# Performance work log

Measured on AMD Instinct MI355X. Metric: run time of the kernel, lower is better.

The kernel has to match this reference:

```python
import jax, jax.numpy as jnp
import numpy as np

B, N, K = 4, 8192, 32
C_IN, C_MID, C_OUT = 64, 64, 128


def _uniform(key, shape, fan_in):
    s = 1.0 / np.sqrt(fan_in).astype(np.float32)
    return jax.random.uniform(key, shape, minval=-s, maxval=s, dtype=jnp.float32)


def setup_inputs() -> dict:
    key = jax.random.key(0)
    ks = jax.random.split(key, 8)
    p = jax.random.normal(ks[0], (B, N, 3), dtype=jnp.float32)
    f = jax.random.normal(ks[1], (B, C_IN, N), dtype=jnp.float32)
    dp = jax.random.normal(ks[2], (B, 3, N, K), dtype=jnp.float32)
    fj = jax.random.normal(ks[3], (B, C_IN, N, K), dtype=jnp.float32)
    # Conv2d 1x1 weights (PyTorch default kaiming-uniform-ish fan-in init)
    W1 = _uniform(ks[4], (C_MID, C_IN + 3), C_IN + 3)
    b1 = _uniform(ks[5], (C_MID,), C_IN + 3)
    W2 = _uniform(ks[6], (C_OUT, C_MID), C_MID)
    b2 = _uniform(ks[7], (C_OUT,), C_MID)
    return {"p": p, "f": f, "dp": dp, "fj": fj, "W1": W1, "b1": b1, "W2": W2, "b2": b2}


def reference(p, f, dp, fj, W1, b1, W2, b2):
    # fj <- cat([dp, fj], dim=1): [B, 3+C_in, N, K]
    x = jnp.concatenate([dp, fj], axis=1)
    # 1x1 Conv2d + ReLU (norm is None in source), layer 1: [B, C_mid, N, K]
    h = jax.nn.relu(jnp.einsum('oc,bcnk->bonk', W1, x) + b1[None, :, None, None])
    # layer 2 (use_res=False, is_head=False -> ReLU on last layer too): [B, C_out, N, K]
    h = jax.nn.relu(jnp.einsum('oc,bcnk->bonk', W2, h) + b2[None, :, None, None])
    # max-pool over neighbor axis K: [B, C_out, N]
    return jnp.max(h, axis=-1)
```

## Files before the change

### kernel.cpp

```cpp
#include <hip/hip_runtime.h>
#include <hip/hip_bf16.h>
#include <stdint.h>

#define B_    4
#define N_    8192
#define K_    32
#define CX    67
#define CMID  64
#define COUT  128

#define CSTR  100
#define HSTR  72
#define TPG   8
#define NWG   1024

typedef __bf16 bf16_t;
typedef bf16_t bf16x8 __attribute__((ext_vector_type(8)));
typedef bf16_t bf16x4 __attribute__((ext_vector_type(4)));
typedef float  f32x4  __attribute__((ext_vector_type(4)));

__device__ __forceinline__ uint32_t pack2bf(float a, float b) {
    union { bf16_t h[2]; uint32_t u; } x;
    x.h[0] = (bf16_t)a; x.h[1] = (bf16_t)b;
    return x.u;
}

template<bool DIRECT>
__global__ __launch_bounds__(256, 2)
void sa_main(const float* __restrict__ dp, const float* __restrict__ fj,
             const float* __restrict__ W1, const float* __restrict__ b1,
             const float* __restrict__ W2, const float* __restrict__ b2,
             float* __restrict__ dst)
{
    __shared__ bf16_t smem[4 * 32 * CSTR + 4 * 16 * HSTR];

    const int tid  = threadIdx.x;
    const int wave = tid >> 6;
    const int lane = tid & 63;
    const int lrow = lane & 15;
    const int g    = lane >> 4;

    bf16_t* Xw = smem + wave * 32 * CSTR;
    bf16_t* Hw = smem + 4 * 32 * CSTR + wave * 16 * HSTR;

    const size_t plane = (size_t)N_ * K_;
    const int cr = lane >> 3;
    const int k0 = (lane & 7) << 2;

    float4 v[9];
    auto issue = [&](int Gi) {
        const int bb = Gi >> 11;
        const int nn = ((Gi & 2047) << 2) + wave;
        const size_t rbase = (size_t)nn * K_ + k0;
        const float* dpb = dp + (size_t)bb * 3  * plane + rbase;
        const float* fjb = fj + (size_t)bb * 64 * plane + rbase;
        #pragma unroll
        for (int j = 0; j < 9; ++j) {
            int c = j * 8 + cr;
            int cc = (c < CX) ? c : (CX - 1);
            const float* p = (cc < 3) ? dpb + (size_t)cc * plane
                                      : fjb + (size_t)(cc - 3) * plane;
            v[j] = *(const float4*)p;
        }
    };
    issue(blockIdx.x * TPG);

    for (int i = tid; i < 64 * 96; i += 256) {
        int o = i / 96, c = i - o * 96;
        smem[i] = (c < CX) ? (bf16_t)W1[o * CX + c] : (bf16_t)0.f;
    }
    __syncthreads();
    bf16x8 w1f[3][4];
    #pragma unroll
    for (int kc = 0; kc < 3; ++kc)
        #pragma unroll
        for (int rt = 0; rt < 4; ++rt)
            w1f[kc][rt] = *(const bf16x8*)&smem[(rt * 16 + lrow) * 96 + kc * 32 + g * 8];
    __syncthreads();
    for (int i = tid; i < 128 * 72; i += 256) {
        int o = i / 72, c = i - o * 72;
        smem[i] = (c < CMID) ? (bf16_t)W2[o * CMID + c] : (bf16_t)0.f;
    }
    __syncthreads();
    bf16x8 w2f[2][8];
    #pragma unroll
    for (int kc = 0; kc < 2; ++kc)
        #pragma unroll
        for (int ot = 0; ot < 8; ++ot)
            w2f[kc][ot] = *(const bf16x8*)&smem[(ot * 16 + lrow) * 72 + kc * 32 + g * 8];
    __syncthreads();
    for (int i = tid; i < 4 * 32 * CSTR; i += 256) smem[i] = (bf16_t)0.f;
    __syncthreads();

    f32x4 b1f[4];
    #pragma unroll
    for (int rt = 0; rt < 4; ++rt) b1f[rt] = *(const f32x4*)(b1 + rt * 16 + g * 4);
    float b2f[8];
    #pragma unroll
    for (int ot = 0; ot < 8; ++ot) b2f[ot] = b2[ot * 16 + lrow];

    #pragma unroll 1
    for (int t = 0; t < TPG; ++t) {
        const int G = blockIdx.x * TPG + t;
        const int b = G >> 11;
        const int n = ((G & 2047) << 2) + wave;

        #pragma unroll
        for (int j = 0; j < 9; ++j) {
            int c = j * 8 + cr;
            if (c < CX) {
                Xw[(k0 + 0) * CSTR + c] = (bf16_t)v[j].x;
                Xw[(k0 + 1) * CSTR + c] = (bf16_t)v[j].y;
                Xw[(k0 + 2) * CSTR + c] = (bf16_t)v[j].z;
                Xw[(k0 + 3) * CSTR + c] = (bf16_t)v[j].w;
            }
        }
        {
            int Gn = G + 1;
            if (Gn > 8191) Gn = 8191;
            issue(Gn);
        }

        float macc[8];
        #pragma unroll
        for (int i = 0; i < 8; ++i) macc[i] = -3e38f;

        #pragma unroll
        for (int ct = 0; ct < 2; ++ct) {
            const int col = ct * 16 + lrow;
            f32x4 acc1[4] = {};
            #pragma unroll
            for (int kc = 0; kc < 3; ++kc) {
                bf16x4 lo = *(const bf16x4*)&Xw[col * CSTR + kc * 32 + g * 8];
                bf16x4 hi = *(const bf16x4*)&Xw[col * CSTR + kc * 32 + g * 8 + 4];
                bf16x8 bfX = __builtin_shufflevector(lo, hi, 0, 1, 2, 3, 4, 5, 6, 7);
                #pragma unroll
                for (int rt = 0; rt < 4; ++rt)
                    acc1[rt] = __builtin_amdgcn_mfma_f32_16x16x32_bf16(w1f[kc][rt], bfX, acc1[rt], 0, 0, 0);
            }
            #pragma unroll
            for (int rt = 0; rt < 4; ++rt) {
                float h0 = fmaxf(acc1[rt][0] + b1f[rt][0], 0.f);
                float h1 = fmaxf(acc1[rt][1] + b1f[rt][1], 0.f);
                float h2 = fmaxf(acc1[rt][2] + b1f[rt][2], 0.f);
                float h3 = fmaxf(acc1[rt][3] + b1f[rt][3], 0.f);
                *(uint2*)&Hw[lrow * HSTR + rt * 16 + g * 4] =
                    make_uint2(pack2bf(h0, h1), pack2bf(h2, h3));
            }
            bf16x8 hb0 = *(const bf16x8*)&Hw[lrow * HSTR +  0 + g * 8];
            bf16x8 hb1 = *(const bf16x8*)&Hw[lrow * HSTR + 32 + g * 8];
            #pragma unroll
            for (int bt = 0; bt < 2; ++bt) {
                f32x4 a2[4] = {};
                #pragma unroll
                for (int o = 0; o < 4; ++o) {
                    a2[o] = __builtin_amdgcn_mfma_f32_16x16x32_bf16(hb0, w2f[0][bt * 4 + o], a2[o], 0, 0, 0);
                    a2[o] = __builtin_amdgcn_mfma_f32_16x16x32_bf16(hb1, w2f[1][bt * 4 + o], a2[o], 0, 0, 0);
                }
                #pragma unroll
                for (int o = 0; o < 4; ++o) {
                    float m = fmaxf(fmaxf(a2[o][0], a2[o][1]), fmaxf(a2[o][2], a2[o][3]));
                    macc[bt * 4 + o] = fmaxf(macc[bt * 4 + o], m);
                }
            }
        }

        #pragma unroll
        for (int ot = 0; ot < 8; ++ot) {
            float vv = macc[ot];
            vv = fmaxf(vv, __shfl_xor(vv, 16, 64));
            vv = fmaxf(vv, __shfl_xor(vv, 32, 64));
            macc[ot] = fmaxf(vv + b2f[ot], 0.f);
        }
        float va = (g == 0) ? macc[0] : (g == 1) ? macc[2] : (g == 2) ? macc[4] : macc[6];
        float vb = (g == 0) ? macc[1] : (g == 1) ? macc[3] : (g == 2) ? macc[5] : macc[7];
        const int ca = g * 32 + lrow;
        const int cb = g * 32 + 16 + lrow;
        if (DIRECT) {
            float* op = dst + (size_t)b * COUT * N_ + n;
            op[(size_t)ca * N_] = va;
            op[(size_t)cb * N_] = vb;
        } else {
            float* wp = dst + ((size_t)(b * N_ + n)) * COUT;
            wp[ca] = va;
            wp[cb] = vb;
        }
    }
}

__global__ __launch_bounds__(256)
void sa_transpose(const float* __restrict__ ws, float* __restrict__ out)
{
    __shared__ float tile[32][136];
    const int t  = threadIdx.x;
    const int i  = blockIdx.x;
    const int b  = i >> 8;
    const int n0 = (i & 255) << 5;

    const float* rp = ws + ((size_t)(b * N_ + n0)) * COUT;
    #pragma unroll
    for (int r = 0; r < 4; ++r) {
        int flat = (r * 256 + t) * 4;
        int nl = flat >> 7, c = flat & 127;
        float4 v = *(const float4*)(rp + (size_t)nl * COUT + c);
        *(float4*)&tile[nl][c] = v;
    }
    __syncthreads();
    float* op = out + (size_t)b * COUT * N_ + n0;
    const int nl4 = (t & 7) << 2;
    #pragma unroll
    for (int r2 = 0; r2 < 4; ++r2) {
        int c = r2 * 32 + (t >> 3);
        float4 o4;
        o4.x = tile[nl4 + 0][c];
        o4.y = tile[nl4 + 1][c];
        o4.z = tile[nl4 + 2][c];
        o4.w = tile[nl4 + 3][c];
        *(float4*)(op + (size_t)c * N_ + nl4) = o4;
    }
}

extern "C" void kernel_launch(void* const* d_in, const int* in_sizes, int n_in,
                              void* d_out, int out_size, void* d_ws, size_t ws_size,
                              hipStream_t stream) {
    const float* dp = (const float*)d_in[2];
    const float* fj = (const float*)d_in[3];
    const float* W1 = (const float*)d_in[4];
    const float* b1 = (const float*)d_in[5];
    const float* W2 = (const float*)d_in[6];
    const float* b2 = (const float*)d_in[7];
    float* out = (float*)d_out;

    const size_t ws_need = (size_t)B_ * N_ * COUT * sizeof(float);
    if (ws_size >= ws_need) {
        float* ws = (float*)d_ws;
        hipLaunchKernelGGL((sa_main<false>), dim3(NWG), dim3(256), 0, stream,
                           dp, fj, W1, b1, W2, b2, ws);
        hipLaunchKernelGGL(sa_transpose, dim3(1024), dim3(256), 0, stream, ws, out);
    } else {
        hipLaunchKernelGGL((sa_main<true>), dim3(NWG), dim3(256), 0, stream,
                           dp, fj, W1, b1, W2, b2, out);
    }
}
```

Measured before the change: 111.3 us.

## Double-buffer global loads two points ahead and add MFMA wave priority

The kernel now keeps two register buffers of input loads and prefetches two points ahead instead of one, so more global memory latency can be hidden behind MFMA work. The per-channel load address computation is simplified into strided pointer increments instead of per-element selects. s_setprio is raised around the MFMA blocks. The extra register buffer raises VGPR pressure, which at launch bounds 256,2 may cause spills.

Result: slower. 115.0 us (+3.3%).

```diff
diff --git a/kernel.cpp b/kernel.cpp
--- a/kernel.cpp
+++ b/kernel.cpp
@@ -13,6 +13,7 @@
 #define HSTR  72
 #define TPG   8
 #define NWG   1024
+#define GMAX  8191
 
 typedef __bf16 bf16_t;
 typedef bf16_t bf16x8 __attribute__((ext_vector_type(8)));
@@ -47,23 +48,31 @@
     const int cr = lane >> 3;
     const int k0 = (lane & 7) << 2;
 
-    float4 v[9];
-    auto issue = [&](int Gi) {
+    auto issue = [&](float4 (&v)[9], int Gi) {
         const int bb = Gi >> 11;
         const int nn = ((Gi & 2047) << 2) + wave;
         const size_t rbase = (size_t)nn * K_ + k0;
-        const float* dpb = dp + (size_t)bb * 3  * plane + rbase;
-        const float* fjb = fj + (size_t)bb * 64 * plane + rbase;
-        #pragma unroll
-        for (int j = 0; j < 9; ++j) {
-            int c = j * 8 + cr;
-            int cc = (c < CX) ? c : (CX - 1);
-            const float* p = (cc < 3) ? dpb + (size_t)cc * plane
-                                      : fjb + (size_t)(cc - 3) * plane;
-            v[j] = *(const float4*)p;
-        }
+        const float* fp  = fj + (size_t)bb * 64 * plane + rbase;
+        const float* dp0 = dp + (size_t)bb * 3  * plane + rbase;
+        const float* p0 = (cr < 3) ? dp0 + (size_t)cr * plane
+                                   : fp  + (size_t)(cr - 3) * plane;
+        v[0] = *(const float4*)p0;
+        const float* pj = fp + (size_t)(8 + cr - 3) * plane;
+        #pragma unroll
+        for (int j = 1; j < 8; ++j) {
+            v[j] = *(const float4*)pj;
+            pj += 8 * plane;
+        }
+        const int c8 = (cr < 3) ? (64 + cr) : 66;
+        v[8] = *(const float4*)(fp + (size_t)(c8 - 3) * plane);
     };
-    issue(blockIdx.x * TPG);
+
+    float4 va[9], vb[9];
+    {
+        const int G0 = blockIdx.x * TPG;
+        issue(va, G0);
+        issue(vb, G0 + 1 > GMAX ? GMAX : G0 + 1);
+    }
 
     for (int i = tid; i < 64 * 96; i += 256) {
         int o = i / 96, c = i - o * 96;
@@ -99,9 +108,7 @@
     #pragma unroll
     for (int ot = 0; ot < 8; ++ot) b2f[ot] = b2[ot * 16 + lrow];
 
-    #pragma unroll 1
-    for (int t = 0; t < TPG; ++t) {
-        const int G = blockIdx.x * TPG + t;
+    auto point = [&](float4 (&v)[9], int G) {
         const int b = G >> 11;
         const int n = ((G & 2047) << 2) + wave;
 
@@ -116,9 +123,9 @@
             }
         }
         {
-            int Gn = G + 1;
-            if (Gn > 8191) Gn = 8191;
-            issue(Gn);
+            int Gn = G + 2;
+            if (Gn > GMAX) Gn = GMAX;
+            issue(v, Gn);
         }
 
         float macc[8];
@@ -129,6 +136,7 @@
         for (int ct = 0; ct < 2; ++ct) {
             const int col = ct * 16 + lrow;
             f32x4 acc1[4] = {};
+            __builtin_amdgcn_s_setprio(1);
             #pragma unroll
             for (int kc = 0; kc < 3; ++kc) {
                 bf16x4 lo = *(const bf16x4*)&Xw[col * CSTR + kc * 32 + g * 8];
@@ -138,6 +146,7 @@
                 for (int rt = 0; rt < 4; ++rt)
                     acc1[rt] = __builtin_amdgcn_mfma_f32_16x16x32_bf16(w1f[kc][rt], bfX, acc1[rt], 0, 0, 0);
             }
+            __builtin_amdgcn_s_setprio(0);
             #pragma unroll
             for (int rt = 0; rt < 4; ++rt) {
                 float h0 = fmaxf(acc1[rt][0] + b1f[rt][0], 0.f);
@@ -149,6 +158,7 @@
             }
             bf16x8 hb0 = *(const bf16x8*)&Hw[lrow * HSTR +  0 + g * 8];
             bf16x8 hb1 = *(const bf16x8*)&Hw[lrow * HSTR + 32 + g * 8];
+            __builtin_amdgcn_s_setprio(1);
             #pragma unroll
             for (int bt = 0; bt < 2; ++bt) {
                 f32x4 a2[4] = {};
@@ -163,6 +173,7 @@
                     macc[bt * 4 + o] = fmaxf(macc[bt * 4 + o], m);
                 }
             }
+            __builtin_amdgcn_s_setprio(0);
         }
 
         #pragma unroll
@@ -172,19 +183,26 @@
             vv = fmaxf(vv, __shfl_xor(vv, 32, 64));
             macc[ot] = fmaxf(vv + b2f[ot], 0.f);
         }
-        float va = (g == 0) ? macc[0] : (g == 1) ? macc[2] : (g == 2) ? macc[4] : macc[6];
-        float vb = (g == 0) ? macc[1] : (g == 1) ? macc[3] : (g == 2) ? macc[5] : macc[7];
+        float oa = (g == 0) ? macc[0] : (g == 1) ? macc[2] : (g == 2) ? macc[4] : macc[6];
+        float ob = (g == 0) ? macc[1] : (g == 1) ? macc[3] : (g == 2) ? macc[5] : macc[7];
         const int ca = g * 32 + lrow;
         const int cb = g * 32 + 16 + lrow;
         if (DIRECT) {
             float* op = dst + (size_t)b * COUT * N_ + n;
-            op[(size_t)ca * N_] = va;
-            op[(size_t)cb * N_] = vb;
+            op[(size_t)ca * N_] = oa;
+            op[(size_t)cb * N_] = ob;
         } else {
             float* wp = dst + ((size_t)(b * N_ + n)) * COUT;
-            wp[ca] = va;
-            wp[cb] = vb;
-        }
+            wp[ca] = oa;
+            wp[cb] = ob;
+        }
+    };
+
+    #pragma unroll 1
+    for (int t = 0; t < TPG; t += 2) {
+        const int G = blockIdx.x * TPG + t;
+        point(va, G);
+        point(vb, G + 1);
     }
 }
 
```
